# Kernel optimization log

Hardware: AMD Instinct MI355X
Metric: run time of the kernel (lower is better)

The kernel has to match this reference:

```python
import jax, jax.numpy as jnp
import numpy as np

N_NODES = 100000


def _gcn_conv(x, edge_index, W, b):
    # edge_index: [2, E] (src, dst). PyG GCNConv: add self-loops, symmetric norm.
    n = x.shape[0]
    src = jnp.concatenate([edge_index[0], jnp.arange(n, dtype=edge_index.dtype)])
    dst = jnp.concatenate([edge_index[1], jnp.arange(n, dtype=edge_index.dtype)])
    deg = jax.ops.segment_sum(jnp.ones_like(dst, dtype=x.dtype), dst, num_segments=n)
    dinv = jnp.where(deg > 0, jax.lax.rsqrt(deg), 0.0)
    norm = dinv[src] * dinv[dst]                      # [E+N]
    h = x @ W                                         # transform first (small dim)
    msg = h[src] * norm[:, None]                      # gather + normalize
    out = jax.ops.segment_sum(msg, dst, num_segments=n)  # scatter-aggregate
    return out + b


def setup_inputs() -> dict:
    key = jax.random.key(0)
    ks = jax.random.split(key, 8)
    x = jax.random.normal(ks[0], (N_NODES, 128), dtype=jnp.float32)
    edge_index = jax.random.randint(ks[1], (2, 1600000), 0, N_NODES, dtype=jnp.int32)
    def glorot(k, shape):
        lim = float(np.sqrt(6.0 / (shape[0] + shape[1])))
        return jax.random.uniform(k, shape, jnp.float32, -lim, lim)
    return {
        "x": x,
        "edge_index": edge_index,
        "W1": glorot(ks[2], (128, 64)),
        "b1": jnp.zeros((64,), jnp.float32),
        "W2": glorot(ks[3], (64, 64)),
        "b2": jnp.zeros((64,), jnp.float32),
        "Wh": glorot(ks[4], (64, 40)),
        "bh": jnp.zeros((40,), jnp.float32),
    }


def reference(x, edge_index, W1, b1, W2, b2, Wh, bh):
    # eval mode: dropout is identity
    h = jax.nn.relu(_gcn_conv(x, edge_index, W1, b1))
    h = jax.nn.relu(_gcn_conv(h, edge_index, W2, b2))
    return h @ Wh + bh  # [N, num_classes]
```

## Files before the change

kernel.cpp:

```cpp
#include <hip/hip_runtime.h>
#include <hip/hip_bf16.h>


#define BIN_SHIFT 9
#define BN        (1 << BIN_SHIFT)
#define NB_MAX    256
#define BIN_CHUNK 4096

typedef __attribute__((ext_vector_type(8))) short short8v;
typedef __attribute__((ext_vector_type(4))) float f32x4;

__device__ __forceinline__ float bf2f(unsigned short u) {
  union { unsigned i; float f; } c; c.i = ((unsigned)u) << 16; return c.f;
}
__device__ __forceinline__ unsigned short f2bf(float f) {
  union { float f; unsigned i; } c; c.f = f;
  unsigned r = c.i + 0x7FFFu + ((c.i >> 16) & 1u);
  return (unsigned short)(r >> 16);
}

__global__ __launch_bounds__(256) void k_zero(int* p, int n) {
  int i = blockIdx.x * blockDim.x + threadIdx.x;
  if (i < n) p[i] = 0;
}

__global__ __launch_bounds__(64) void k_zrow(unsigned short* hs, int n) {
  if (threadIdx.x < 32) ((unsigned*)(hs + (size_t)n * 64))[threadIdx.x] = 0u;
}

__global__ __launch_bounds__(256) void k_bhist(const int* __restrict__ dst,
                                               int* bhist, int E, int nb) {
  __shared__ int lh[NB_MAX];
  lh[threadIdx.x] = 0;
  __syncthreads();
  for (int i = blockIdx.x * 256 + threadIdx.x; i < E; i += gridDim.x * 256)
    atomicAdd(&lh[dst[i] >> BIN_SHIFT], 1);
  __syncthreads();
  int v = lh[threadIdx.x];
  if (threadIdx.x < nb && v) atomicAdd(&bhist[threadIdx.x], v);
}

__global__ __launch_bounds__(256) void k_bscan(const int* __restrict__ bhist,
                                               int* boff, int* gcur, int nb, int E) {
  __shared__ int sh[256];
  const int t = threadIdx.x;
  int v = (t < nb) ? bhist[t] : 0;
  sh[t] = v;
  __syncthreads();
  for (int d = 1; d < 256; d <<= 1) {
    int x = (t >= d) ? sh[t - d] : 0;
    __syncthreads();
    sh[t] += x;
    __syncthreads();
  }
  if (t < nb) { int e = sh[t] - v; boff[t] = e; gcur[t] = e; }
  if (t == 0) boff[nb] = E;
}

__global__ __launch_bounds__(256) void k_bin(
    const int* __restrict__ src, const int* __restrict__ dst,
    int* gcur, int* __restrict__ binned, int E)
{
  __shared__ int  hist[NB_MAX];
  __shared__ int  excl[NB_MAX];
  __shared__ int  lcur[NB_MAX];
  __shared__ int  gbase[NB_MAX];
  __shared__ int2 stage[BIN_CHUNK];

  const int t = threadIdx.x;
  const int base = blockIdx.x * BIN_CHUNK;
  const int m = min(BIN_CHUNK, E - base);

  int2 pr[BIN_CHUNK / 256];
  int nmine = 0;
  #pragma unroll
  for (int i = 0; i < BIN_CHUNK / 256; ++i) {
    int idx = t + 256 * i;
    if (idx < m) {
      pr[i].x = src[base + idx];
      pr[i].y = dst[base + idx];
      nmine = i + 1;
    }
  }

  hist[t] = 0;
  __syncthreads();
  #pragma unroll
  for (int i = 0; i < BIN_CHUNK / 256; ++i)
    if (i < nmine) atomicAdd(&hist[pr[i].y >> BIN_SHIFT], 1);
  __syncthreads();

  const int mycnt = hist[t];
  for (int d = 1; d < 256; d <<= 1) {
    int v = (t >= d) ? hist[t - d] : 0;
    __syncthreads();
    hist[t] += v;
    __syncthreads();
  }
  {
    int e = hist[t] - mycnt;
    excl[t] = e;
    lcur[t] = e;
    gbase[t] = mycnt ? atomicAdd(&gcur[t], mycnt) : 0;
  }
  __syncthreads();

  #pragma unroll
  for (int i = 0; i < BIN_CHUNK / 256; ++i)
    if (i < nmine) {
      int b = pr[i].y >> BIN_SHIFT;
      int p = atomicAdd(&lcur[b], 1);
      stage[p] = pr[i];
    }
  __syncthreads();

  for (int i = t; i < m; i += 256) {
    int2 pp = stage[i];
    int b = pp.y >> BIN_SHIFT;
    binned[gbase[b] + (i - excl[b])] =
        (pp.x << BIN_SHIFT) | (pp.y & (BN - 1));
  }
}

__global__ __launch_bounds__(256) void k_csr(
    const int* __restrict__ binned, const int* __restrict__ boff,
    int* __restrict__ offs, int* __restrict__ endo,
    float* __restrict__ dinv, int* __restrict__ csr, int n)
{
  __shared__ int cnt_l[BN];
  __shared__ int tsum[256];
  __shared__ int lcur[BN];
  const int t = threadIdx.x;
  const int b = blockIdx.x;
  const int base = boff[b];
  const int end  = boff[b + 1];
  const int n0 = b << BIN_SHIFT;

  cnt_l[t] = 0; cnt_l[t + 256] = 0;
  __syncthreads();
  for (int i = base + t; i < end; i += 256)
    atomicAdd(&cnt_l[binned[i] & (BN - 1)], 1);
  __syncthreads();

  const int c0 = cnt_l[2 * t];
  const int c1 = cnt_l[2 * t + 1];
  const int s = c0 + c1;
  tsum[t] = s;
  __syncthreads();
  for (int d = 1; d < 256; d <<= 1) {
    int v = (t >= d) ? tsum[t - d] : 0;
    __syncthreads();
    tsum[t] += v;
    __syncthreads();
  }
  const int ex = tsum[t] - s;
  const int e0 = ex, e1 = ex + c0;
  const int g0 = n0 + 2 * t, g1 = g0 + 1;
  if (g0 < n) {
    offs[g0] = base + e0; endo[g0] = base + e1;
    dinv[g0] = rsqrtf((float)(c0 + 1));
  }
  if (g1 < n) {
    offs[g1] = base + e1; endo[g1] = base + e1 + c1;
    dinv[g1] = rsqrtf((float)(c1 + 1));
  }
  lcur[2 * t] = e0;
  lcur[2 * t + 1] = e1;
  __syncthreads();
  for (int i = base + t; i < end; i += 256) {
    int v = binned[i];
    int p = atomicAdd(&lcur[v & (BN - 1)], 1);
    csr[base + p] = v >> BIN_SHIFT;
  }
}

__global__ __launch_bounds__(256) void k_count(const int* __restrict__ dst, int* cnt, int E) {
  int e = blockIdx.x * blockDim.x + threadIdx.x;
  if (e < E) atomicAdd(&cnt[dst[e]], 1);
}
__global__ __launch_bounds__(256) void k_dinv(const int* __restrict__ cnt, float* dinv, int n) {
  int i = blockIdx.x * blockDim.x + threadIdx.x;
  if (i < n) dinv[i] = rsqrtf((float)(cnt[i] + 1));
}
__global__ __launch_bounds__(256) void k_scan1(const int* __restrict__ cnt,
                                               int* offs, int* bsum, int n) {
  __shared__ int sh[256];
  const int t = threadIdx.x;
  const int base = blockIdx.x * 1024 + t * 4;
  int v0 = 0, v1 = 0, v2 = 0, v3 = 0;
  if (base + 0 < n) v0 = cnt[base + 0];
  if (base + 1 < n) v1 = cnt[base + 1];
  if (base + 2 < n) v2 = cnt[base + 2];
  if (base + 3 < n) v3 = cnt[base + 3];
  const int s = v0 + v1 + v2 + v3;
  sh[t] = s;
  __syncthreads();
  for (int d = 1; d < 256; d <<= 1) {
    int x = (t >= d) ? sh[t - d] : 0;
    __syncthreads();
    sh[t] += x;
    __syncthreads();
  }
  int o = sh[t] - s;
  if (t == 255) bsum[blockIdx.x] = sh[255];
  if (base + 0 < n) { offs[base + 0] = o; o += v0; }
  if (base + 1 < n) { offs[base + 1] = o; o += v1; }
  if (base + 2 < n) { offs[base + 2] = o; o += v2; }
  if (base + 3 < n) { offs[base + 3] = o; o += v3; }
}
__global__ __launch_bounds__(256) void k_scan2(int* bsum, int nb) {
  __shared__ int sh[256];
  const int t = threadIdx.x;
  int v = (t < nb) ? bsum[t] : 0;
  sh[t] = v;
  __syncthreads();
  for (int d = 1; d < 256; d <<= 1) {
    int x = (t >= d) ? sh[t - d] : 0;
    __syncthreads();
    sh[t] += x;
    __syncthreads();
  }
  if (t < nb) bsum[t] = sh[t] - v;
}
__global__ __launch_bounds__(256) void k_scan3(int* offs, const int* __restrict__ bsum,
                                               int* cursor, int n) {
  int i = blockIdx.x * blockDim.x + threadIdx.x;
  if (i < n) {
    int o = offs[i] + bsum[i >> 10];
    offs[i] = o;
    cursor[i] = o;
  }
}
__global__ __launch_bounds__(256) void k_fill(const int* __restrict__ src,
                                              const int* __restrict__ dst,
                                              int* cursor, int* csr, int E) {
  int e = blockIdx.x * blockDim.x + threadIdx.x;
  if (e < E) {
    int p = atomicAdd(&cursor[dst[e]], 1);
    csr[p] = src[e];
  }
}

template<int K, int NOUT, bool SCALE, bool BIAS, bool OUTBF>
__global__ __launch_bounds__(256) void k_gemm(
    const float* __restrict__ X, const float* __restrict__ W,
    const float* __restrict__ dinv, const float* __restrict__ bias,
    void* __restrict__ Yv, int nrows)
{
  constexpr int NCOL = (NOUT + 15) & ~15;
  constexpr int NT   = NCOL / 16;
  constexpr int KS   = K / 32;
  __shared__ __align__(16) unsigned short Xs[64 * K];
  __shared__ __align__(16) unsigned short WTs[NCOL * K];

  const int t = threadIdx.x;
  const int r0 = blockIdx.x * 64;

  if constexpr (NCOL != NOUT) {
    for (int i = t; i < (NCOL - NOUT) * K; i += 256)
      WTs[NOUT * K + i] = 0;
  }
  for (int idx = t; idx < K * NOUT; idx += 256) {
    int k = idx / NOUT, n = idx - k * NOUT;
    int u = (k >> 3) ^ (n & 7);
    WTs[n * K + u * 8 + (k & 7)] = f2bf(W[idx]);
  }
  for (int q = t; q < 16 * K; q += 256) {
    int row = q / (K / 4);
    int c4  = q - row * (K / 4);
    int gr  = r0 + row; if (gr >= nrows) gr = nrows - 1;
    float4 v = *(const float4*)&X[(size_t)gr * K + c4 * 4];
    int u = (c4 >> 1) ^ (row & 7);
    unsigned short* p = &Xs[row * K + u * 8 + (c4 & 1) * 4];
    p[0] = f2bf(v.x); p[1] = f2bf(v.y); p[2] = f2bf(v.z); p[3] = f2bf(v.w);
  }
  __syncthreads();

  const int wid  = t >> 6;
  const int lane = t & 63;
  const int l15  = lane & 15;
  const int kb   = lane >> 4;
  const int lrow = 16 * wid + l15;

  f32x4 acc[NT];
  #pragma unroll
  for (int j = 0; j < NT; ++j) { f32x4 z = {0.f, 0.f, 0.f, 0.f}; acc[j] = z; }

  #pragma unroll
  for (int ks = 0; ks < KS; ++ks) {
    const int ub = ks * 4 + kb;
    short8v a = *(const short8v*)&Xs[lrow * K + (ub ^ (lrow & 7)) * 8];
    #pragma unroll
    for (int j = 0; j < NT; ++j) {
      const int n = j * 16 + l15;
      short8v b = *(const short8v*)&WTs[n * K + (ub ^ (n & 7)) * 8];
      acc[j] = __builtin_amdgcn_mfma_f32_16x16x32_bf16(a, b, acc[j], 0, 0, 0);
    }
  }

  const int rbase = r0 + 16 * wid + kb * 4;
  #pragma unroll
  for (int r = 0; r < 4; ++r) {
    const int row = rbase + r;
    if (row >= nrows) continue;
    const float sc = SCALE ? dinv[row] : 1.f;
    #pragma unroll
    for (int j = 0; j < NT; ++j) {
      const int col = j * 16 + l15;
      if (col < NOUT) {
        float v = acc[j][r];
        if constexpr (SCALE) v *= sc;
        if constexpr (BIAS)  v += bias[col];
        if constexpr (OUTBF)
          ((unsigned short*)Yv)[(size_t)row * NOUT + col] = f2bf(v);
        else
          ((float*)Yv)[(size_t)row * NOUT + col] = v;
      }
    }
  }
}

__global__ __launch_bounds__(256) void k_pull(
    const unsigned short* __restrict__ hs, const int* __restrict__ csr,
    const int* __restrict__ offs, const int* __restrict__ endo,
    const float* __restrict__ dinv, const float* __restrict__ bias,
    float* __restrict__ out, int n)
{
  const int node = blockIdx.x * 4 + (threadIdx.x >> 6);
  if (node >= n) return;
  const int lane = threadIdx.x & 63;
  const int g    = lane >> 4;
  const int fl   = lane & 15;

  const int beg = offs[node];
  const int m   = endo[node] - beg;
  const int mp  = (m + 3) & ~3;

  float a0 = 0.f, a1 = 0.f, a2 = 0.f, a3 = 0.f;

  for (int base = 0; base < mp; base += 64) {
    const int rem = mp - base;
    const int kk  = rem < 64 ? rem : 64;
    const int myidx = (base + lane < m) ? csr[beg + base + lane] : n;
    const int nq = kk >> 2;
    #pragma unroll 4
    for (int i = 0; i < nq; ++i) {
      int s = __shfl(myidx, 4 * i + g);
      uint2 u = *(const uint2*)&hs[(size_t)s * 64 + fl * 4];
      a0 += bf2f((unsigned short)u.x); a1 += bf2f((unsigned short)(u.x >> 16));
      a2 += bf2f((unsigned short)u.y); a3 += bf2f((unsigned short)(u.y >> 16));
    }
  }

  a0 += __shfl_xor(a0, 16); a1 += __shfl_xor(a1, 16);
  a2 += __shfl_xor(a2, 16); a3 += __shfl_xor(a3, 16);
  a0 += __shfl_xor(a0, 32); a1 += __shfl_xor(a1, 32);
  a2 += __shfl_xor(a2, 32); a3 += __shfl_xor(a3, 32);

  if (lane < 16) {
    uint2 u = *(const uint2*)&hs[(size_t)node * 64 + fl * 4];
    a0 += bf2f((unsigned short)u.x); a1 += bf2f((unsigned short)(u.x >> 16));
    a2 += bf2f((unsigned short)u.y); a3 += bf2f((unsigned short)(u.y >> 16));
    const float dv = dinv[node];
    const float4 bb = *(const float4*)&bias[fl * 4];
    float4 o;
    o.x = fmaxf(fmaf(dv, a0, bb.x), 0.f);
    o.y = fmaxf(fmaf(dv, a1, bb.y), 0.f);
    o.z = fmaxf(fmaf(dv, a2, bb.z), 0.f);
    o.w = fmaxf(fmaf(dv, a3, bb.w), 0.f);
    *(float4*)&out[(size_t)node * 64 + fl * 4] = o;
  }
}

extern "C" void kernel_launch(void* const* d_in, const int* in_sizes, int n_in,
                              void* d_out, int out_size, void* d_ws, size_t ws_size,
                              hipStream_t stream) {
  const float* x  = (const float*)d_in[0];
  const int*   ei = (const int*)d_in[1];
  const float* W1 = (const float*)d_in[2];
  const float* b1 = (const float*)d_in[3];
  const float* W2 = (const float*)d_in[4];
  const float* b2 = (const float*)d_in[5];
  const float* Wh = (const float*)d_in[6];
  const float* bh = (const float*)d_in[7];
  float* out = (float*)d_out;

  const int N = in_sizes[0] / 128;
  const int E = in_sizes[1] / 2;
  const int* src = ei;
  const int* dst = ei + E;

  auto align_up = [](size_t v, size_t a) { return (v + a - 1) & ~(a - 1); };
  char* ws = (char*)d_ws;
  size_t off = 0;
  int*   cnt    = (int*)(ws + off);   off = align_up(off + (size_t)N * 4, 256);
  float* dinv   = (float*)(ws + off); off = align_up(off + (size_t)N * 4, 256);
  int*   offs   = (int*)(ws + off);   off = align_up(off + (size_t)N * 4, 256);
  int*   endo   = (int*)(ws + off);   off = align_up(off + (size_t)N * 4, 256);
  int*   bsum   = (int*)(ws + off);   off = align_up(off + 256 * 4, 256);
  int*   bhist  = (int*)(ws + off);   off = align_up(off + NB_MAX * 4, 256);
  int*   boff   = (int*)(ws + off);   off = align_up(off + (NB_MAX + 1) * 4, 256);
  int*   gcur   = (int*)(ws + off);   off = align_up(off + NB_MAX * 4, 256);
  int*   csr    = (int*)(ws + off);   off = align_up(off + (size_t)E * 4, 256);
  int*   binned = (int*)(ws + off);   off = align_up(off + (size_t)E * 4, 256);
  unsigned short* A = (unsigned short*)(ws + off);
  off = align_up(off + (size_t)(N + 1) * 64 * 2, 256);
  float* B      = (float*)(ws + off); off = align_up(off + (size_t)N * 64 * 4, 256);
  (void)ws_size;

  const int TB = 256;
  const int gN = (N + TB - 1) / TB;
  const int gE = (E + TB - 1) / TB;
  const int NBk = (N + BN - 1) >> BIN_SHIFT;
  const int gGemm = (N + 63) / 64;
  const int gPull = (N + 3) / 4;
  const int gBin  = (E + BIN_CHUNK - 1) / BIN_CHUNK;

  k_zrow<<<1, 64, 0, stream>>>(A, N);

  if (NBk <= NB_MAX) {
    k_zero <<<1, TB, 0, stream>>>(bhist, NBk);
    k_bhist<<<512, TB, 0, stream>>>(dst, bhist, E, NBk);
    k_bscan<<<1, TB, 0, stream>>>(bhist, boff, gcur, NBk, E);
    k_bin  <<<gBin, TB, 0, stream>>>(src, dst, gcur, binned, E);
    k_csr  <<<NBk, TB, 0, stream>>>(binned, boff, offs, endo, dinv, csr, N);
  } else {
    k_zero <<<gN, TB, 0, stream>>>(cnt, N);
    k_count<<<gE, TB, 0, stream>>>(dst, cnt, E);
    k_dinv <<<gN, TB, 0, stream>>>(cnt, dinv, N);
    const int nb1 = (N + 1023) / 1024;
    k_scan1<<<nb1, TB, 0, stream>>>(cnt, offs, bsum, N);
    k_scan2<<<1,  TB, 0, stream>>>(bsum, nb1);
    k_scan3<<<gN, TB, 0, stream>>>(offs, bsum, endo, N);
    k_fill <<<gE, TB, 0, stream>>>(src, dst, endo, csr, E);
  }

  k_gemm<128, 64, true, false, true><<<gGemm, TB, 0, stream>>>(x, W1, dinv, nullptr, A, N);
  k_pull<<<gPull, TB, 0, stream>>>(A, csr, offs, endo, dinv, b1, B, N);

  k_gemm<64, 64, true, false, true><<<gGemm, TB, 0, stream>>>(B, W2, dinv, nullptr, A, N);
  k_pull<<<gPull, TB, 0, stream>>>(A, csr, offs, endo, dinv, b2, B, N);

  k_gemm<64, 40, false, true, false><<<gGemm, TB, 0, stream>>>(B, Wh, nullptr, bh, out, N);
}
```

Before: 204.6 us.

## Store transformed features in 16-column slices and pull per slice

The bf16 feature table written by the GEMM is now laid out as four column slices of 16 features each, each slice a contiguous [N+1,16] array. The pull kernel assigns one slice per block, so each gathered neighbour row for that slice is a 32-byte chunk and a slice's table is a quarter of the full footprint, which should make it easier to keep in cache. Each 16-lane group now handles one node, and csr loads and output stores use nontemporal hints. In exchange, every slice re-reads the CSR index list four times, issues narrower 2-byte loads, and lanes idle when neighbour counts differ within a wave.

```diff
diff --git a/kernel.cpp b/kernel.cpp
--- a/kernel.cpp
+++ b/kernel.cpp
@@ -24,8 +24,12 @@
   if (i < n) p[i] = 0;
 }
 
-__global__ __launch_bounds__(64) void k_zrow(unsigned short* hs, int n) {
-  if (threadIdx.x < 32) ((unsigned*)(hs + (size_t)n * 64))[threadIdx.x] = 0u;
+__global__ __launch_bounds__(64) void k_zrow(unsigned short* hsS, int n) {
+  int t = threadIdx.x;
+  if (t < 64) {
+    int s = t >> 4, f = t & 15;
+    hsS[((size_t)s * (n + 1) + n) * 16 + f] = 0;
+  }
 }
 
 __global__ __launch_bounds__(256) void k_bhist(const int* __restrict__ dst,
@@ -245,7 +249,7 @@
 __global__ __launch_bounds__(256) void k_gemm(
     const float* __restrict__ X, const float* __restrict__ W,
     const float* __restrict__ dinv, const float* __restrict__ bias,
-    void* __restrict__ Yv, int nrows)
+    void* __restrict__ Yv, int nrows, int nstride)
 {
   constexpr int NCOL = (NOUT + 15) & ~15;
   constexpr int NT   = NCOL / 16;
@@ -312,7 +316,7 @@
         if constexpr (SCALE) v *= sc;
         if constexpr (BIAS)  v += bias[col];
         if constexpr (OUTBF)
-          ((unsigned short*)Yv)[(size_t)row * NOUT + col] = f2bf(v);
+          ((unsigned short*)Yv)[((size_t)(col >> 4) * nstride + row) * 16 + (col & 15)] = f2bf(v);
         else
           ((float*)Yv)[(size_t)row * NOUT + col] = v;
       }
@@ -321,54 +325,44 @@
 }
 
 __global__ __launch_bounds__(256) void k_pull(
-    const unsigned short* __restrict__ hs, const int* __restrict__ csr,
+    const unsigned short* __restrict__ hsS, const int* __restrict__ csr,
     const int* __restrict__ offs, const int* __restrict__ endo,
     const float* __restrict__ dinv, const float* __restrict__ bias,
     float* __restrict__ out, int n)
 {
-  const int node = blockIdx.x * 4 + (threadIdx.x >> 6);
-  if (node >= n) return;
-  const int lane = threadIdx.x & 63;
-  const int g    = lane >> 4;
-  const int fl   = lane & 15;
-
-  const int beg = offs[node];
-  const int m   = endo[node] - beg;
-  const int mp  = (m + 3) & ~3;
-
-  float a0 = 0.f, a1 = 0.f, a2 = 0.f, a3 = 0.f;
-
-  for (int base = 0; base < mp; base += 64) {
-    const int rem = mp - base;
-    const int kk  = rem < 64 ? rem : 64;
-    const int myidx = (base + lane < m) ? csr[beg + base + lane] : n;
-    const int nq = kk >> 2;
-    #pragma unroll 4
-    for (int i = 0; i < nq; ++i) {
-      int s = __shfl(myidx, 4 * i + g);
-      uint2 u = *(const uint2*)&hs[(size_t)s * 64 + fl * 4];
-      a0 += bf2f((unsigned short)u.x); a1 += bf2f((unsigned short)(u.x >> 16));
-      a2 += bf2f((unsigned short)u.y); a3 += bf2f((unsigned short)(u.y >> 16));
+  const int b     = blockIdx.x;
+  const int slice = b & 3;
+  const int wid   = threadIdx.x >> 6;
+  const int lane  = threadIdx.x & 63;
+  const int f     = lane & 15;
+  const int node  = (b >> 2) * 16 + wid * 4 + (lane >> 4);
+  const bool valid = node < n;
+  const int nd    = valid ? node : 0;
+
+  const unsigned short* hp = hsS + (size_t)slice * (n + 1) * 16;
+
+  const int beg = offs[nd];
+  const int m   = valid ? (endo[nd] - beg) : 0;
+
+  int mmax = m;
+  mmax = max(mmax, __shfl_xor(mmax, 16));
+  mmax = max(mmax, __shfl_xor(mmax, 32));
+
+  float acc = 0.f;
+  for (int base = 0; base < mmax; base += 16) {
+    int idx = (base + f < m) ? __builtin_nontemporal_load(&csr[beg + base + f]) : n;
+    #pragma unroll
+    for (int i = 0; i < 16; ++i) {
+      int s = __shfl(idx, (lane & 48) + i);
+      acc += bf2f(hp[(size_t)s * 16 + f]);
     }
   }
 
-  a0 += __shfl_xor(a0, 16); a1 += __shfl_xor(a1, 16);
-  a2 += __shfl_xor(a2, 16); a3 += __shfl_xor(a3, 16);
-  a0 += __shfl_xor(a0, 32); a1 += __shfl_xor(a1, 32);
-  a2 += __shfl_xor(a2, 32); a3 += __shfl_xor(a3, 32);
-
-  if (lane < 16) {
-    uint2 u = *(const uint2*)&hs[(size_t)node * 64 + fl * 4];
-    a0 += bf2f((unsigned short)u.x); a1 += bf2f((unsigned short)(u.x >> 16));
-    a2 += bf2f((unsigned short)u.y); a3 += bf2f((unsigned short)(u.y >> 16));
-    const float dv = dinv[node];
-    const float4 bb = *(const float4*)&bias[fl * 4];
-    float4 o;
-    o.x = fmaxf(fmaf(dv, a0, bb.x), 0.f);
-    o.y = fmaxf(fmaf(dv, a1, bb.y), 0.f);
-    o.z = fmaxf(fmaf(dv, a2, bb.z), 0.f);
-    o.w = fmaxf(fmaf(dv, a3, bb.w), 0.f);
-    *(float4*)&out[(size_t)node * 64 + fl * 4] = o;
+  if (valid) {
+    acc += bf2f(hp[(size_t)nd * 16 + f]);
+    float v = fmaf(dinv[nd], acc, bias[slice * 16 + f]);
+    __builtin_nontemporal_store(fmaxf(v, 0.f),
+                                &out[(size_t)nd * 64 + slice * 16 + f]);
   }
 }
 
@@ -413,8 +407,9 @@
   const int gE = (E + TB - 1) / TB;
   const int NBk = (N + BN - 1) >> BIN_SHIFT;
   const int gGemm = (N + 63) / 64;
-  const int gPull = (N + 3) / 4;
+  const int gPull = ((N + 15) / 16) * 4;
   const int gBin  = (E + BIN_CHUNK - 1) / BIN_CHUNK;
+  const int NS = N + 1;
 
   k_zrow<<<1, 64, 0, stream>>>(A, N);
 
@@ -435,11 +430,11 @@
     k_fill <<<gE, TB, 0, stream>>>(src, dst, endo, csr, E);
   }
 
-  k_gemm<128, 64, true, false, true><<<gGemm, TB, 0, stream>>>(x, W1, dinv, nullptr, A, N);
+  k_gemm<128, 64, true, false, true><<<gGemm, TB, 0, stream>>>(x, W1, dinv, nullptr, A, N, NS);
   k_pull<<<gPull, TB, 0, stream>>>(A, csr, offs, endo, dinv, b1, B, N);
 
-  k_gemm<64, 64, true, false, true><<<gGemm, TB, 0, stream>>>(B, W2, dinv, nullptr, A, N);
+  k_gemm<64, 64, true, false, true><<<gGemm, TB, 0, stream>>>(B, W2, dinv, nullptr, A, N, NS);
   k_pull<<<gPull, TB, 0, stream>>>(A, csr, offs, endo, dinv, b2, B, N);
 
-  k_gemm<64, 40, false, true, false><<<gGemm, TB, 0, stream>>>(B, Wh, nullptr, bh, out, N);
-}
+  k_gemm<64, 40, false, true, false><<<gGemm, TB, 0, stream>>>(B, Wh, nullptr, bh, out, N, 0);
+}
```

Result: slower. 245.0 us (+19.8%).
